# Optimization experiments

Hardware: AMD Instinct MI355X
Metric: run time of the kernel (lower is better)

Reference implementation:

```python
import jax, jax.numpy as jnp
import numpy as np

# Filter defaults from the torch module
SCORE_THR = 0.05
IOU_THR = 0.5
MAX_DET = 300
K_PRE = 512          # candidate pool for fixed-size NMS (>= MAX_DET)
BBOX_STD = jnp.array([0.1, 0.1, 0.2, 0.2], dtype=jnp.float32)  # retinanet-style bbox_transform_inv std
IMG = 800.0


def setup_inputs() -> dict:
    key = jax.random.key(0)
    k1, k2, k3, k4 = jax.random.split(key, 4)
    B, N, C = 8, 200000, 80
    # valid xyxy anchors: centers in [0, 800], sizes in [16, 256]
    ctr = jax.random.uniform(k1, (B, N, 2), dtype=jnp.float32) * IMG
    wh = 16.0 + jax.random.uniform(k2, (B, N, 2), dtype=jnp.float32) * 240.0
    anchors = jnp.concatenate([ctr - 0.5 * wh, ctr + 0.5 * wh], axis=-1)
    reg = jax.random.normal(k3, (B, N, 4), dtype=jnp.float32)
    cls = jax.random.uniform(k4, (B, N, C), dtype=jnp.float32)
    sizes = jnp.full((B, 2), IMG, dtype=jnp.float32)  # (h, w) per image
    return {"anchors": anchors, "reg": reg, "cls": cls, "sizes": sizes}


def bbox_transform_inv(anchors, reg):
    # anchors, reg: [B, N, 4] xyxy / deltas
    w = anchors[..., 2] - anchors[..., 0]
    h = anchors[..., 3] - anchors[..., 1]
    cx = anchors[..., 0] + 0.5 * w
    cy = anchors[..., 1] + 0.5 * h
    dx, dy, dw, dh = (reg * BBOX_STD)[..., 0], (reg * BBOX_STD)[..., 1], (reg * BBOX_STD)[..., 2], (reg * BBOX_STD)[..., 3]
    pcx = cx + dx * w
    pcy = cy + dy * h
    pw = jnp.exp(dw) * w
    ph = jnp.exp(dh) * h
    return jnp.stack([pcx - 0.5 * pw, pcy - 0.5 * ph, pcx + 0.5 * pw, pcy + 0.5 * ph], axis=-1)


def clip_boxes(bbox, sizes):
    # ClipBoxes: x coords clipped to [0, w=sizes[:,1]], y coords to [0, h=sizes[:,0]]
    w = sizes[:, 1][:, None]
    h = sizes[:, 0][:, None]
    x1 = jnp.clip(bbox[..., 0], 0.0, w)
    y1 = jnp.clip(bbox[..., 1], 0.0, h)
    x2 = jnp.clip(bbox[..., 2], 0.0, w)
    y2 = jnp.clip(bbox[..., 3], 0.0, h)
    return jnp.stack([x1, y1, x2, y2], axis=-1)


def pairwise_iou(b):
    # b: [K, 4] -> [K, K]
    area = (b[:, 2] - b[:, 0]) * (b[:, 3] - b[:, 1])
    lt = jnp.maximum(b[:, None, :2], b[None, :, :2])
    rb = jnp.minimum(b[:, None, 2:], b[None, :, 2:])
    wh = jnp.clip(rb - lt, 0.0)
    inter = wh[..., 0] * wh[..., 1]
    return inter / (area[:, None] + area[None, :] - inter + 1e-9)


def greedy_nms_keep(boxes, valid):
    # boxes: [K, 4] already sorted by descending score; valid: [K] bool
    K = boxes.shape[0]
    iou = pairwise_iou(boxes)
    idx = jnp.arange(K)
    def body(i, keep):
        sup = (iou[i] > IOU_THR) & (idx > i) & keep[i]
        return keep & ~sup
    keep = jax.lax.fori_loop(0, K, body, valid)
    return keep


def filter_one(boxes, scores, labels):
    # boxes [N,4], scores [N], labels [N] -> padded (MAX_DET) outputs, pad = -1
    masked = jnp.where(scores > SCORE_THR, scores, -jnp.inf)
    top_s, top_i = jax.lax.top_k(masked, K_PRE)          # sorted descending
    cand_b = boxes[top_i]                                 # [K_PRE, 4]
    cand_l = labels[top_i]
    cand_valid = top_s > SCORE_THR
    keep = greedy_nms_keep(cand_b, cand_valid)
    kept_s = jnp.where(keep, top_s, -jnp.inf)
    det_s, det_i = jax.lax.top_k(kept_s, MAX_DET)
    det_b = cand_b[det_i]
    det_l = cand_l[det_i]
    ok = det_s > -jnp.inf
    out_b = jnp.where(ok[:, None], det_b, -1.0)
    out_s = jnp.where(ok, det_s, -1.0)[:, None]
    out_l = jnp.where(ok, det_l.astype(jnp.float32), -1.0)[:, None]
    return out_b, out_s, out_l


def reference(anchors, reg, cls, sizes):
    bbox = bbox_transform_inv(anchors, reg)   # [B, N, 4]
    bbox = clip_boxes(bbox, sizes)
    scores = jnp.max(cls, axis=-1)            # class_specific_filter=False path
    labels = jnp.argmax(cls, axis=-1)
    select_boxes, select_scores, select_labels = jax.vmap(filter_one)(bbox, scores, labels)
    return select_boxes, select_scores, select_labels
```

## Files before the change

### kernel.cpp

```cpp
#include <hip/hip_runtime.h>
#include <hip/hip_bf16.h>
#include <math.h>

#define KPRE 512
#define CAP 4096
#define MAXDET 300
#define SCORE_THR 0.05f
#define IOU_THR 0.5f
#define NREP 16

__device__ __forceinline__ unsigned key_bin(unsigned key) {
    return (key >> 10) & 0xFFFFu;
}

template<int F4A>
__global__ __launch_bounds__(256)
void score_label_kernel(const float* __restrict__ cls,
                        unsigned* __restrict__ keys,
                        unsigned char* __restrict__ labels,
                        int N) {
    const int b = blockIdx.y;
    const int tid = threadIdx.x;
    const int g = tid >> 2, q = tid & 3;
    const int a = blockIdx.x * 64 + g;
    if (a >= N) return;
    const float4* p = (const float4*)cls + ((size_t)b * N + a) * F4A;

    float4 vv[F4A / 4];
#pragma unroll
    for (int j = 0; j < F4A / 4; ++j) vv[j] = p[q + 4 * j];

    unsigned long long best = 0ull;
#pragma unroll
    for (int j = 0; j < F4A / 4; ++j) {
        float4 v = vv[j];
        int cbase = (q + 4 * j) * 4;
        float m = v.x; int c = cbase;
        if (v.y > m) { m = v.y; c = cbase + 1; }
        if (v.z > m) { m = v.z; c = cbase + 2; }
        if (v.w > m) { m = v.w; c = cbase + 3; }
        unsigned long long comp =
            ((unsigned long long)__float_as_uint(m) << 32) | (unsigned)(255 - c);
        if (comp > best) best = comp;
    }
    unsigned long long o;
    o = (unsigned long long)__shfl_xor((long long)best, 1, 64); if (o > best) best = o;
    o = (unsigned long long)__shfl_xor((long long)best, 2, 64); if (o > best) best = o;

    if (q == 0) {
        unsigned sb = (unsigned)(best >> 32);
        unsigned cl = 255u - (unsigned)(best & 0xFFFFFFFFull);
        size_t idx = (size_t)b * N + a;
        keys[idx] = (__uint_as_float(sb) > SCORE_THR) ? sb : 0u;
        labels[idx] = (unsigned char)cl;
    }
}

__global__ __launch_bounds__(256)
void score_label_generic(const float* __restrict__ cls,
                         unsigned* __restrict__ keys,
                         unsigned char* __restrict__ labels,
                         int N, int C) {
    const int b = blockIdx.y;
    const int tid = threadIdx.x;
    const int g = tid >> 2, q = tid & 3;
    const int a = blockIdx.x * 64 + g;
    if (a >= N) return;
    const int F4A = C >> 2;
    const float4* p = (const float4*)cls + ((size_t)b * N + a) * F4A;
    unsigned long long best = 0ull;
    for (int f4 = q; f4 < F4A; f4 += 4) {
        float4 v = p[f4];
        int cbase = f4 * 4;
        float m = v.x; int c = cbase;
        if (v.y > m) { m = v.y; c = cbase + 1; }
        if (v.z > m) { m = v.z; c = cbase + 2; }
        if (v.w > m) { m = v.w; c = cbase + 3; }
        unsigned long long comp =
            ((unsigned long long)__float_as_uint(m) << 32) | (unsigned)(255 - c);
        if (comp > best) best = comp;
    }
    unsigned long long o;
    o = (unsigned long long)__shfl_xor((long long)best, 1, 64); if (o > best) best = o;
    o = (unsigned long long)__shfl_xor((long long)best, 2, 64); if (o > best) best = o;
    if (q == 0) {
        unsigned sb = (unsigned)(best >> 32);
        unsigned cl = 255u - (unsigned)(best & 0xFFFFFFFFull);
        size_t idx = (size_t)b * N + a;
        keys[idx] = (__uint_as_float(sb) > SCORE_THR) ? sb : 0u;
        labels[idx] = (unsigned char)cl;
    }
}

__global__ __launch_bounds__(1024, 1)
void select_nms_kernel(const float* __restrict__ anchors,
                       const float* __restrict__ reg,
                       const float* __restrict__ sizes,
                       const unsigned* __restrict__ keys,
                       const unsigned char* __restrict__ labels,
                       float* __restrict__ out,
                       int N, int B) {
    const int b = blockIdx.x;
    const int tid = threadIdx.x;
    const int nthr = blockDim.x;

    __shared__ __align__(16) unsigned long long buf[CAP];
    unsigned* lhist = (unsigned*)buf;
    unsigned* sup = (unsigned*)buf;
    __shared__ float4 boxs[KPRE];
    __shared__ float areas[KPRE];
    __shared__ unsigned ckey[KPRE];
    __shared__ unsigned cidx[KPRE];
    __shared__ unsigned sscan[256];
    __shared__ unsigned validw[16], keepw_s[16], wpref[17];
    __shared__ unsigned sh_cnt, sh_above, sh_H;
    __shared__ int sh_H1, sh_M;

    const unsigned* kb = keys + (size_t)b * N;
    const uint4* k4 = (const uint4*)kb;
    const int N4 = N >> 2;
    const unsigned rrep = (tid & (NREP - 1)) * 256;

    if (tid == 0) { sh_H1 = -1; sh_cnt = 0; sh_H = 1; }

    for (int i = tid; i < 256 * NREP; i += nthr) lhist[i] = 0;
    __syncthreads();
    for (int i = tid; i < N4; i += nthr) {
        uint4 v = k4[i];
        if (v.x) atomicAdd(&lhist[rrep + (key_bin(v.x) >> 8)], 1u);
        if (v.y) atomicAdd(&lhist[rrep + (key_bin(v.y) >> 8)], 1u);
        if (v.z) atomicAdd(&lhist[rrep + (key_bin(v.z) >> 8)], 1u);
        if (v.w) atomicAdd(&lhist[rrep + (key_bin(v.w) >> 8)], 1u);
    }
    for (int i = (N4 << 2) + tid; i < N; i += nthr) {
        unsigned kk = kb[i];
        if (kk) atomicAdd(&lhist[rrep + (key_bin(kk) >> 8)], 1u);
    }
    __syncthreads();
    if (tid < 256) {
        unsigned s = 0;
        for (int j = 0; j < NREP; ++j) s += lhist[j * 256 + tid];
        sscan[tid] = s;
    }
    __syncthreads();
    for (int off = 1; off < 256; off <<= 1) {
        unsigned v2 = 0;
        if (tid < 256) v2 = sscan[tid] + ((tid + off < 256) ? sscan[tid + off] : 0u);
        __syncthreads();
        if (tid < 256) sscan[tid] = v2;
        __syncthreads();
    }
    if (tid < 256) {
        unsigned above = (tid < 255) ? sscan[tid + 1] : 0u;
        if (sscan[tid] >= KPRE && above < KPRE) { sh_H1 = tid; sh_above = above; }
    }
    __syncthreads();

    const int H1 = sh_H1;
    unsigned H = 1;
    if (H1 >= 0) {
        for (int i = tid; i < 256 * NREP; i += nthr) lhist[i] = 0;
        __syncthreads();
        for (int i = tid; i < N4; i += nthr) {
            uint4 v = k4[i];
            unsigned fb;
            if (v.x) { fb = key_bin(v.x); if ((int)(fb >> 8) == H1) atomicAdd(&lhist[rrep + (fb & 255u)], 1u); }
            if (v.y) { fb = key_bin(v.y); if ((int)(fb >> 8) == H1) atomicAdd(&lhist[rrep + (fb & 255u)], 1u); }
            if (v.z) { fb = key_bin(v.z); if ((int)(fb >> 8) == H1) atomicAdd(&lhist[rrep + (fb & 255u)], 1u); }
            if (v.w) { fb = key_bin(v.w); if ((int)(fb >> 8) == H1) atomicAdd(&lhist[rrep + (fb & 255u)], 1u); }
        }
        for (int i = (N4 << 2) + tid; i < N; i += nthr) {
            unsigned kk = kb[i];
            if (kk) { unsigned fb = key_bin(kk); if ((int)(fb >> 8) == H1) atomicAdd(&lhist[rrep + (fb & 255u)], 1u); }
        }
        __syncthreads();
        if (tid < 256) {
            unsigned s = 0;
            for (int j = 0; j < NREP; ++j) s += lhist[j * 256 + tid];
            sscan[tid] = s;
        }
        __syncthreads();
        for (int off = 1; off < 256; off <<= 1) {
            unsigned v2 = 0;
            if (tid < 256) v2 = sscan[tid] + ((tid + off < 256) ? sscan[tid + off] : 0u);
            __syncthreads();
            if (tid < 256) sscan[tid] = v2;
            __syncthreads();
        }
        if (tid < 256) {
            unsigned abv = ((tid < 255) ? sscan[tid + 1] : 0u) + sh_above;
            if (sscan[tid] + sh_above >= KPRE && abv < KPRE) sh_H = ((unsigned)H1 << 8) + tid;
        }
        __syncthreads();
        H = sh_H; if (H == 0) H = 1;
    }

    for (int i = tid; i < N4; i += nthr) {
        uint4 v = k4[i];
        unsigned base = (unsigned)(i << 2);
        if (key_bin(v.x) >= H) { unsigned p = atomicAdd(&sh_cnt, 1u); if (p < CAP) buf[p] = ((unsigned long long)v.x << 32) | ~(base); }
        if (key_bin(v.y) >= H) { unsigned p = atomicAdd(&sh_cnt, 1u); if (p < CAP) buf[p] = ((unsigned long long)v.y << 32) | ~(base + 1u); }
        if (key_bin(v.z) >= H) { unsigned p = atomicAdd(&sh_cnt, 1u); if (p < CAP) buf[p] = ((unsigned long long)v.z << 32) | ~(base + 2u); }
        if (key_bin(v.w) >= H) { unsigned p = atomicAdd(&sh_cnt, 1u); if (p < CAP) buf[p] = ((unsigned long long)v.w << 32) | ~(base + 3u); }
    }
    for (int i = (N4 << 2) + tid; i < N; i += nthr) {
        unsigned kk = kb[i];
        if (key_bin(kk) >= H) { unsigned p = atomicAdd(&sh_cnt, 1u); if (p < CAP) buf[p] = ((unsigned long long)kk << 32) | ~((unsigned)i); }
    }
    __syncthreads();
    int cnt = (int)sh_cnt; if (cnt > CAP) cnt = CAP;
    if (tid == 0) {
        int M = KPRE;
        while (M < cnt) M <<= 1;
        sh_M = M;
    }
    __syncthreads();
    const int M = sh_M;
    for (int i2 = cnt + tid; i2 < M; i2 += nthr) buf[i2] = 0ull;
    __syncthreads();

    for (int kk = 2; kk <= M; kk <<= 1) {
        for (int j = kk >> 1; j > 0; j >>= 1) {
            for (int i2 = tid; i2 < M; i2 += nthr) {
                int l = i2 ^ j;
                if (l > i2) {
                    unsigned long long a = buf[i2], c = buf[l];
                    bool desc = ((i2 & kk) == 0);
                    if (desc ? (a < c) : (a > c)) { buf[i2] = c; buf[l] = a; }
                }
            }
            __syncthreads();
        }
    }

    const float wimg = sizes[b * 2 + 1];
    const float himg = sizes[b * 2 + 0];
    for (int t = tid; t < KPRE; t += nthr) {
        unsigned long long c = buf[t];
        unsigned key = (unsigned)(c >> 32);
        unsigned ai = ~(unsigned)(c & 0xFFFFFFFFull);
        bool valid = (key != 0u) && (t < cnt);
        ckey[t] = valid ? key : 0u;
        cidx[t] = valid ? ai : 0u;
        float4 bx = make_float4(0.f, 0.f, 0.f, 0.f);
        if (valid) {
            const float4 a4 = *(const float4*)(anchors + ((size_t)b * N + ai) * 4);
            const float4 r4 = *(const float4*)(reg + ((size_t)b * N + ai) * 4);
            float w = a4.z - a4.x, h = a4.w - a4.y;
            float cx = a4.x + 0.5f * w, cy = a4.y + 0.5f * h;
            float dx = r4.x * 0.1f, dy = r4.y * 0.1f;
            float dw = r4.z * 0.2f, dh = r4.w * 0.2f;
            float pcx = cx + dx * w, pcy = cy + dy * h;
            float pw = expf(dw) * w, ph = expf(dh) * h;
            float x1 = pcx - 0.5f * pw, y1 = pcy - 0.5f * ph;
            float x2 = pcx + 0.5f * pw, y2 = pcy + 0.5f * ph;
            bx.x = fminf(fmaxf(x1, 0.f), wimg);
            bx.y = fminf(fmaxf(y1, 0.f), himg);
            bx.z = fminf(fmaxf(x2, 0.f), wimg);
            bx.w = fminf(fmaxf(y2, 0.f), himg);
        }
        boxs[t] = bx;
        areas[t] = (bx.z - bx.x) * (bx.w - bx.y);
    }
    __syncthreads();

    for (int unit = tid; unit < KPRE * 16; unit += nthr) {
        int i = unit >> 4, w = unit & 15;
        float4 bi = boxs[i];
        float ai = areas[i];
        unsigned bits = 0;
        int j0 = w * 32;
        for (int bit = 0; bit < 32; ++bit) {
            int j = j0 + bit;
            if (j > i) {
                float4 bj = boxs[j];
                float ltx = fmaxf(bi.x, bj.x), lty = fmaxf(bi.y, bj.y);
                float rbx = fminf(bi.z, bj.z), rby = fminf(bi.w, bj.w);
                float iw = fmaxf(rbx - ltx, 0.f), ih = fmaxf(rby - lty, 0.f);
                float inter = iw * ih;
                float iou = inter / (ai + areas[j] - inter + 1e-9f);
                if (iou > IOU_THR) bits |= (1u << bit);
            }
        }
        sup[i * 16 + w] = bits;
    }
    __syncthreads();

    unsigned long long bal = __ballot(tid < KPRE && ckey[tid] != 0u);
    if (tid < KPRE && (tid & 63) == 0) {
        validw[(tid >> 6) * 2] = (unsigned)(bal & 0xFFFFFFFFull);
        validw[(tid >> 6) * 2 + 1] = (unsigned)(bal >> 32);
    }
    __syncthreads();

    if (tid < 64) {
        unsigned kw = (tid < 16) ? validw[tid] : 0u;
        for (int i = 0; i < KPRE; ++i) {
            unsigned rw = sup[i * 16 + (tid & 15)];
            unsigned ow = __shfl(kw, i >> 5, 64);
            if ((ow >> (i & 31)) & 1u) kw &= ~rw;
        }
        if (tid < 16) keepw_s[tid] = kw;
    }
    __syncthreads();

    if (tid == 0) {
        unsigned s = 0;
        for (int w2 = 0; w2 < 16; ++w2) { wpref[w2] = s; s += __popc(keepw_s[w2]); }
        wpref[16] = s;
    }
    __syncthreads();
    const unsigned nk = wpref[16];

    float* ob = out;
    float* os = out + (size_t)B * MAXDET * 4;
    float* ol = os + (size_t)B * MAXDET;
    const unsigned char* lb = labels + (size_t)b * N;

    for (int t = tid; t < KPRE; t += nthr) {
        unsigned word = keepw_s[t >> 5];
        if ((word >> (t & 31)) & 1u) {
            unsigned rank = wpref[t >> 5] + __popc(word & ((1u << (t & 31)) - 1u));
            if (rank < MAXDET) {
                float4 bx = boxs[t];
                size_t ro = (size_t)b * MAXDET + rank;
                ob[ro * 4 + 0] = bx.x;
                ob[ro * 4 + 1] = bx.y;
                ob[ro * 4 + 2] = bx.z;
                ob[ro * 4 + 3] = bx.w;
                os[ro] = __uint_as_float(ckey[t]);
                ol[ro] = (float)lb[cidx[t]];
            }
        }
    }
    for (int r = tid; r < MAXDET; r += nthr) {
        if (r >= (int)nk) {
            size_t ro = (size_t)b * MAXDET + r;
            ob[ro * 4 + 0] = -1.f;
            ob[ro * 4 + 1] = -1.f;
            ob[ro * 4 + 2] = -1.f;
            ob[ro * 4 + 3] = -1.f;
            os[ro] = -1.f;
            ol[ro] = -1.f;
        }
    }
}

extern "C" void kernel_launch(void* const* d_in, const int* in_sizes, int n_in,
                              void* d_out, int out_size, void* d_ws, size_t ws_size,
                              hipStream_t stream) {
    const float* anchors = (const float*)d_in[0];
    const float* reg     = (const float*)d_in[1];
    const float* cls     = (const float*)d_in[2];
    const float* sizes   = (const float*)d_in[3];

    const int B = in_sizes[3] / 2;
    const int N = in_sizes[0] / (4 * B);
    const int C = in_sizes[2] / (B * N);
    const int total = B * N;

    unsigned* keys = (unsigned*)d_ws;
    unsigned char* labels = (unsigned char*)((char*)d_ws + (size_t)total * 4);
    float* out = (float*)d_out;

    dim3 blkA(256);
    dim3 grdA((N + 63) / 64, B);
    if (C == 80)
        score_label_kernel<20><<<grdA, blkA, 0, stream>>>(cls, keys, labels, N);
    else
        score_label_generic<<<grdA, blkA, 0, stream>>>(cls, keys, labels, N, C);

    select_nms_kernel<<<dim3(B), dim3(1024), 0, stream>>>(anchors, reg, sizes, keys, labels, out, N, B);
}
```

Baseline: 906.2 us.

## Split per-image radix select into multi-block histogram, threshold and collect kernels

```diff
diff --git a/kernel.cpp b/kernel.cpp
--- a/kernel.cpp
+++ b/kernel.cpp
@@ -8,6 +8,7 @@
 #define SCORE_THR 0.05f
 #define IOU_THR 0.5f
 #define NREP 16
+#define NSEL 32
 
 __device__ __forceinline__ unsigned key_bin(unsigned key) {
     return (key >> 10) & 0xFFFFu;
@@ -92,123 +93,190 @@
     }
 }
 
+__global__ __launch_bounds__(256)
+void init_kernel(unsigned* __restrict__ ghist1, unsigned* __restrict__ ghist2,
+                 int* __restrict__ gmeta, unsigned* __restrict__ gH,
+                 unsigned* __restrict__ gcnt, int B) {
+    const int t = blockIdx.x * 256 + threadIdx.x;
+    if (t < B * 256) { ghist1[t] = 0u; ghist2[t] = 0u; }
+    if (t < B) { gmeta[2 * t] = -1; gmeta[2 * t + 1] = 0; gH[t] = 1u; gcnt[t] = 0u; }
+}
+
+__global__ __launch_bounds__(256)
+void hist_coarse_kernel(const unsigned* __restrict__ keys,
+                        unsigned* __restrict__ ghist1, int N) {
+    const int b = blockIdx.y, tid = threadIdx.x;
+    __shared__ unsigned h[NREP * 256];
+    for (int i = tid; i < NREP * 256; i += 256) h[i] = 0u;
+    __syncthreads();
+    const unsigned rrep = (tid & (NREP - 1)) * 256;
+    const unsigned* kb = keys + (size_t)b * N;
+    const uint4* k4 = (const uint4*)kb;
+    const int N4 = N >> 2;
+    for (int i = blockIdx.x * 256 + tid; i < N4; i += 256 * NSEL) {
+        uint4 v = k4[i];
+        if (v.x) atomicAdd(&h[rrep + (key_bin(v.x) >> 8)], 1u);
+        if (v.y) atomicAdd(&h[rrep + (key_bin(v.y) >> 8)], 1u);
+        if (v.z) atomicAdd(&h[rrep + (key_bin(v.z) >> 8)], 1u);
+        if (v.w) atomicAdd(&h[rrep + (key_bin(v.w) >> 8)], 1u);
+    }
+    if (blockIdx.x == 0) {
+        for (int i = (N4 << 2) + tid; i < N; i += 256) {
+            unsigned kk = kb[i];
+            if (kk) atomicAdd(&h[rrep + (key_bin(kk) >> 8)], 1u);
+        }
+    }
+    __syncthreads();
+    unsigned s = 0;
+    for (int j = 0; j < NREP; ++j) s += h[j * 256 + tid];
+    if (s) atomicAdd(&ghist1[b * 256 + tid], s);
+}
+
+__global__ __launch_bounds__(256)
+void thresh1_kernel(const unsigned* __restrict__ ghist1, int* __restrict__ gmeta) {
+    const int b = blockIdx.x, tid = threadIdx.x;
+    __shared__ unsigned sscan[256];
+    sscan[tid] = ghist1[b * 256 + tid];
+    __syncthreads();
+    for (int off = 1; off < 256; off <<= 1) {
+        unsigned v = sscan[tid] + ((tid + off < 256) ? sscan[tid + off] : 0u);
+        __syncthreads();
+        sscan[tid] = v;
+        __syncthreads();
+    }
+    unsigned above = (tid < 255) ? sscan[tid + 1] : 0u;
+    if (sscan[tid] >= KPRE && above < KPRE) {
+        gmeta[2 * b] = tid;
+        gmeta[2 * b + 1] = (int)above;
+    }
+}
+
+__global__ __launch_bounds__(256)
+void hist_fine_kernel(const unsigned* __restrict__ keys,
+                      const int* __restrict__ gmeta,
+                      unsigned* __restrict__ ghist2, int N) {
+    const int b = blockIdx.y, tid = threadIdx.x;
+    const int h1 = gmeta[2 * b];
+    if (h1 < 0) return;
+    __shared__ unsigned h[NREP * 256];
+    for (int i = tid; i < NREP * 256; i += 256) h[i] = 0u;
+    __syncthreads();
+    const unsigned rrep = (tid & (NREP - 1)) * 256;
+    const unsigned* kb = keys + (size_t)b * N;
+    const uint4* k4 = (const uint4*)kb;
+    const int N4 = N >> 2;
+    for (int i = blockIdx.x * 256 + tid; i < N4; i += 256 * NSEL) {
+        uint4 v = k4[i];
+        unsigned fb;
+        if (v.x) { fb = key_bin(v.x); if ((int)(fb >> 8) == h1) atomicAdd(&h[rrep + (fb & 255u)], 1u); }
+        if (v.y) { fb = key_bin(v.y); if ((int)(fb >> 8) == h1) atomicAdd(&h[rrep + (fb & 255u)], 1u); }
+        if (v.z) { fb = key_bin(v.z); if ((int)(fb >> 8) == h1) atomicAdd(&h[rrep + (fb & 255u)], 1u); }
+        if (v.w) { fb = key_bin(v.w); if ((int)(fb >> 8) == h1) atomicAdd(&h[rrep + (fb & 255u)], 1u); }
+    }
+    if (blockIdx.x == 0) {
+        for (int i = (N4 << 2) + tid; i < N; i += 256) {
+            unsigned kk = kb[i];
+            if (kk) { unsigned fb = key_bin(kk); if ((int)(fb >> 8) == h1) atomicAdd(&h[rrep + (fb & 255u)], 1u); }
+        }
+    }
+    __syncthreads();
+    unsigned s = 0;
+    for (int j = 0; j < NREP; ++j) s += h[j * 256 + tid];
+    if (s) atomicAdd(&ghist2[b * 256 + tid], s);
+}
+
+__global__ __launch_bounds__(256)
+void thresh2_kernel(const unsigned* __restrict__ ghist2,
+                    const int* __restrict__ gmeta, unsigned* __restrict__ gH) {
+    const int b = blockIdx.x, tid = threadIdx.x;
+    const int h1 = gmeta[2 * b];
+    if (h1 < 0) return;
+    const unsigned above = (unsigned)gmeta[2 * b + 1];
+    __shared__ unsigned sscan[256];
+    sscan[tid] = ghist2[b * 256 + tid];
+    __syncthreads();
+    for (int off = 1; off < 256; off <<= 1) {
+        unsigned v = sscan[tid] + ((tid + off < 256) ? sscan[tid + off] : 0u);
+        __syncthreads();
+        sscan[tid] = v;
+        __syncthreads();
+    }
+    unsigned abv = ((tid < 255) ? sscan[tid + 1] : 0u) + above;
+    if (sscan[tid] + above >= KPRE && abv < KPRE) {
+        unsigned H = ((unsigned)h1 << 8) + (unsigned)tid;
+        gH[b] = H ? H : 1u;
+    }
+}
+
+__device__ __forceinline__ void emit_cand(unsigned key, unsigned idx, unsigned H,
+                                          unsigned long long* __restrict__ cand,
+                                          unsigned* __restrict__ cnt, int lane) {
+    bool m = key_bin(key) >= H;
+    unsigned long long mk = __ballot(m);
+    if (!mk) return;
+    int leader = __ffsll(mk) - 1;
+    unsigned basep = 0;
+    if (lane == leader) basep = atomicAdd(cnt, (unsigned)__popcll(mk));
+    basep = (unsigned)__shfl((int)basep, leader, 64);
+    if (m) {
+        unsigned p = basep + (unsigned)__popcll(mk & ((1ull << lane) - 1ull));
+        if (p < CAP) cand[p] = ((unsigned long long)key << 32) | ~idx;
+    }
+}
+
+__global__ __launch_bounds__(256)
+void collect_kernel(const unsigned* __restrict__ keys,
+                    const unsigned* __restrict__ gH,
+                    unsigned long long* __restrict__ gcand,
+                    unsigned* __restrict__ gcnt, int N) {
+    const int b = blockIdx.y, tid = threadIdx.x;
+    const int lane = tid & 63;
+    const unsigned H = gH[b];
+    const unsigned* kb = keys + (size_t)b * N;
+    const uint4* k4 = (const uint4*)kb;
+    const int N4 = N >> 2;
+    unsigned long long* cand = gcand + (size_t)b * CAP;
+    unsigned* cnt = gcnt + b;
+    for (int i = blockIdx.x * 256 + tid; i < N4; i += 256 * NSEL) {
+        uint4 v = k4[i];
+        unsigned base = (unsigned)(i << 2);
+        emit_cand(v.x, base, H, cand, cnt, lane);
+        emit_cand(v.y, base + 1u, H, cand, cnt, lane);
+        emit_cand(v.z, base + 2u, H, cand, cnt, lane);
+        emit_cand(v.w, base + 3u, H, cand, cnt, lane);
+    }
+    if (blockIdx.x == 0) {
+        for (int i = (N4 << 2) + tid; i < N; i += 256)
+            emit_cand(kb[i], (unsigned)i, H, cand, cnt, lane);
+    }
+}
+
 __global__ __launch_bounds__(1024, 1)
-void select_nms_kernel(const float* __restrict__ anchors,
-                       const float* __restrict__ reg,
-                       const float* __restrict__ sizes,
-                       const unsigned* __restrict__ keys,
-                       const unsigned char* __restrict__ labels,
-                       float* __restrict__ out,
-                       int N, int B) {
+void final_nms_kernel(const float* __restrict__ anchors,
+                      const float* __restrict__ reg,
+                      const float* __restrict__ sizes,
+                      const unsigned char* __restrict__ labels,
+                      const unsigned long long* __restrict__ gcand,
+                      const unsigned* __restrict__ gcnt,
+                      float* __restrict__ out,
+                      int N, int B) {
     const int b = blockIdx.x;
     const int tid = threadIdx.x;
     const int nthr = blockDim.x;
 
     __shared__ __align__(16) unsigned long long buf[CAP];
-    unsigned* lhist = (unsigned*)buf;
     unsigned* sup = (unsigned*)buf;
     __shared__ float4 boxs[KPRE];
     __shared__ float areas[KPRE];
     __shared__ unsigned ckey[KPRE];
     __shared__ unsigned cidx[KPRE];
-    __shared__ unsigned sscan[256];
     __shared__ unsigned validw[16], keepw_s[16], wpref[17];
-    __shared__ unsigned sh_cnt, sh_above, sh_H;
-    __shared__ int sh_H1, sh_M;
-
-    const unsigned* kb = keys + (size_t)b * N;
-    const uint4* k4 = (const uint4*)kb;
-    const int N4 = N >> 2;
-    const unsigned rrep = (tid & (NREP - 1)) * 256;
-
-    if (tid == 0) { sh_H1 = -1; sh_cnt = 0; sh_H = 1; }
-
-    for (int i = tid; i < 256 * NREP; i += nthr) lhist[i] = 0;
-    __syncthreads();
-    for (int i = tid; i < N4; i += nthr) {
-        uint4 v = k4[i];
-        if (v.x) atomicAdd(&lhist[rrep + (key_bin(v.x) >> 8)], 1u);
-        if (v.y) atomicAdd(&lhist[rrep + (key_bin(v.y) >> 8)], 1u);
-        if (v.z) atomicAdd(&lhist[rrep + (key_bin(v.z) >> 8)], 1u);
-        if (v.w) atomicAdd(&lhist[rrep + (key_bin(v.w) >> 8)], 1u);
-    }
-    for (int i = (N4 << 2) + tid; i < N; i += nthr) {
-        unsigned kk = kb[i];
-        if (kk) atomicAdd(&lhist[rrep + (key_bin(kk) >> 8)], 1u);
-    }
-    __syncthreads();
-    if (tid < 256) {
-        unsigned s = 0;
-        for (int j = 0; j < NREP; ++j) s += lhist[j * 256 + tid];
-        sscan[tid] = s;
-    }
-    __syncthreads();
-    for (int off = 1; off < 256; off <<= 1) {
-        unsigned v2 = 0;
-        if (tid < 256) v2 = sscan[tid] + ((tid + off < 256) ? sscan[tid + off] : 0u);
-        __syncthreads();
-        if (tid < 256) sscan[tid] = v2;
-        __syncthreads();
-    }
-    if (tid < 256) {
-        unsigned above = (tid < 255) ? sscan[tid + 1] : 0u;
-        if (sscan[tid] >= KPRE && above < KPRE) { sh_H1 = tid; sh_above = above; }
-    }
-    __syncthreads();
-
-    const int H1 = sh_H1;
-    unsigned H = 1;
-    if (H1 >= 0) {
-        for (int i = tid; i < 256 * NREP; i += nthr) lhist[i] = 0;
-        __syncthreads();
-        for (int i = tid; i < N4; i += nthr) {
-            uint4 v = k4[i];
-            unsigned fb;
-            if (v.x) { fb = key_bin(v.x); if ((int)(fb >> 8) == H1) atomicAdd(&lhist[rrep + (fb & 255u)], 1u); }
-            if (v.y) { fb = key_bin(v.y); if ((int)(fb >> 8) == H1) atomicAdd(&lhist[rrep + (fb & 255u)], 1u); }
-            if (v.z) { fb = key_bin(v.z); if ((int)(fb >> 8) == H1) atomicAdd(&lhist[rrep + (fb & 255u)], 1u); }
-            if (v.w) { fb = key_bin(v.w); if ((int)(fb >> 8) == H1) atomicAdd(&lhist[rrep + (fb & 255u)], 1u); }
-        }
-        for (int i = (N4 << 2) + tid; i < N; i += nthr) {
-            unsigned kk = kb[i];
-            if (kk) { unsigned fb = key_bin(kk); if ((int)(fb >> 8) == H1) atomicAdd(&lhist[rrep + (fb & 255u)], 1u); }
-        }
-        __syncthreads();
-        if (tid < 256) {
-            unsigned s = 0;
-            for (int j = 0; j < NREP; ++j) s += lhist[j * 256 + tid];
-            sscan[tid] = s;
-        }
-        __syncthreads();
-        for (int off = 1; off < 256; off <<= 1) {
-            unsigned v2 = 0;
-            if (tid < 256) v2 = sscan[tid] + ((tid + off < 256) ? sscan[tid + off] : 0u);
-            __syncthreads();
-            if (tid < 256) sscan[tid] = v2;
-            __syncthreads();
-        }
-        if (tid < 256) {
-            unsigned abv = ((tid < 255) ? sscan[tid + 1] : 0u) + sh_above;
-            if (sscan[tid] + sh_above >= KPRE && abv < KPRE) sh_H = ((unsigned)H1 << 8) + tid;
-        }
-        __syncthreads();
-        H = sh_H; if (H == 0) H = 1;
-    }
-
-    for (int i = tid; i < N4; i += nthr) {
-        uint4 v = k4[i];
-        unsigned base = (unsigned)(i << 2);
-        if (key_bin(v.x) >= H) { unsigned p = atomicAdd(&sh_cnt, 1u); if (p < CAP) buf[p] = ((unsigned long long)v.x << 32) | ~(base); }
-        if (key_bin(v.y) >= H) { unsigned p = atomicAdd(&sh_cnt, 1u); if (p < CAP) buf[p] = ((unsigned long long)v.y << 32) | ~(base + 1u); }
-        if (key_bin(v.z) >= H) { unsigned p = atomicAdd(&sh_cnt, 1u); if (p < CAP) buf[p] = ((unsigned long long)v.z << 32) | ~(base + 2u); }
-        if (key_bin(v.w) >= H) { unsigned p = atomicAdd(&sh_cnt, 1u); if (p < CAP) buf[p] = ((unsigned long long)v.w << 32) | ~(base + 3u); }
-    }
-    for (int i = (N4 << 2) + tid; i < N; i += nthr) {
-        unsigned kk = kb[i];
-        if (key_bin(kk) >= H) { unsigned p = atomicAdd(&sh_cnt, 1u); if (p < CAP) buf[p] = ((unsigned long long)kk << 32) | ~((unsigned)i); }
-    }
-    __syncthreads();
-    int cnt = (int)sh_cnt; if (cnt > CAP) cnt = CAP;
+    __shared__ int sh_M;
+
+    int cnt = (int)gcnt[b];
+    if (cnt > CAP) cnt = CAP;
+    const unsigned long long* cand = gcand + (size_t)b * CAP;
+    for (int i = tid; i < cnt; i += nthr) buf[i] = cand[i];
     if (tid == 0) {
         int M = KPRE;
         while (M < cnt) M <<= 1;
@@ -359,8 +427,19 @@
     const int C = in_sizes[2] / (B * N);
     const int total = B * N;
 
-    unsigned* keys = (unsigned*)d_ws;
-    unsigned char* labels = (unsigned char*)((char*)d_ws + (size_t)total * 4);
+    char* ws = (char*)d_ws;
+    size_t off = 0;
+    unsigned* keys = (unsigned*)(ws + off);            off += (size_t)total * 4;
+    unsigned char* labels = (unsigned char*)(ws + off); off += (size_t)total;
+    off = (off + 255) & ~(size_t)255;
+    unsigned* ghist1 = (unsigned*)(ws + off);          off += (size_t)B * 256 * 4;
+    unsigned* ghist2 = (unsigned*)(ws + off);          off += (size_t)B * 256 * 4;
+    int* gmeta = (int*)(ws + off);                     off += (size_t)B * 2 * 4;
+    unsigned* gH = (unsigned*)(ws + off);              off += (size_t)B * 4;
+    unsigned* gcnt = (unsigned*)(ws + off);            off += (size_t)B * 4;
+    off = (off + 255) & ~(size_t)255;
+    unsigned long long* gcand = (unsigned long long*)(ws + off);
+
     float* out = (float*)d_out;
 
     dim3 blkA(256);
@@ -370,5 +449,11 @@
     else
         score_label_generic<<<grdA, blkA, 0, stream>>>(cls, keys, labels, N, C);
 
-    select_nms_kernel<<<dim3(B), dim3(1024), 0, stream>>>(anchors, reg, sizes, keys, labels, out, N, B);
-}
+    init_kernel<<<dim3((B * 256 + 255) / 256), dim3(256), 0, stream>>>(ghist1, ghist2, gmeta, gH, gcnt, B);
+    hist_coarse_kernel<<<dim3(NSEL, B), dim3(256), 0, stream>>>(keys, ghist1, N);
+    thresh1_kernel<<<dim3(B), dim3(256), 0, stream>>>(ghist1, gmeta);
+    hist_fine_kernel<<<dim3(NSEL, B), dim3(256), 0, stream>>>(keys, gmeta, ghist2, N);
+    thresh2_kernel<<<dim3(B), dim3(256), 0, stream>>>(ghist2, gmeta, gH);
+    collect_kernel<<<dim3(NSEL, B), dim3(256), 0, stream>>>(keys, gH, gcand, gcnt, N);
+    final_nms_kernel<<<dim3(B), dim3(1024), 0, stream>>>(anchors, reg, sizes, labels, gcand, gcnt, out, N, B);
+}
```

Result: no change. 908.5 us (+0.3%).
